# Kernel optimization log

Hardware: AMD Instinct MI355X
Metric: run time of the kernel (lower is better)

## Reference

```python
import jax, jax.numpy as jnp
import numpy as np
from jax.scipy.special import erfinv

N, F0, F1 = 256, 128, 64          # nodes, scalar channels, vector channels
RB, KSEQ, EMB = 32, 16, 32        # radial bins, seq window, pos-embed dim
RC = 24.0                         # radial_cut
NI = F0 + F1                      # num output irreps (per-irrep scalar gate)
CIN = F0 + F1 + 1 + F0            # 321 = per-l fan-in of the message Linear

# real l=2 CG matrices, e3nn component order: (xz, xy, y^2-(x^2+z^2)/2, yz, z^2-x^2)
_M = np.zeros((5, 3, 3), np.float32)
_M[0, 0, 2] = _M[0, 2, 0] = 1.0 / np.sqrt(10.0)
_M[1, 0, 1] = _M[1, 1, 0] = 1.0 / np.sqrt(10.0)
_M[2] = np.diag([-1.0, 2.0, -1.0]) / np.sqrt(30.0)
_M[3, 1, 2] = _M[3, 2, 1] = 1.0 / np.sqrt(10.0)
_M[4] = np.diag([-1.0, 0.0, 1.0]) / np.sqrt(10.0)
M2 = jnp.asarray(_M)

# e3nn-style normalized activation: silu / sqrt(E[silu(z)^2]), z ~ N(0,1)
_zs = jnp.sqrt(2.0) * erfinv(jnp.linspace(-1.0 + 1e-6, 1.0 - 1e-6, 100001))
C_SILU = jnp.sqrt(jnp.mean(jax.nn.silu(_zs) ** 2))

def nsilu(x):
    return jax.nn.silu(x) / C_SILU

def setup_inputs() -> dict:
    key = jax.random.key(0)
    ks = jax.random.split(key, 12)
    return {
        "feat": jax.random.normal(ks[0], (N, F0 + 3 * F1), jnp.float32),
        "coord": 8.0 * jax.random.normal(ks[1], (N, 3), jnp.float32),
        "W_msg0": jax.random.normal(ks[2], (CIN, F0), jnp.float32),
        "W_msg1": jax.random.normal(ks[3], (CIN, F1), jnp.float32),
        "embed_tbl": jax.random.normal(ks[4], (2 * KSEQ + 1, EMB), jnp.float32) / jnp.sqrt(2.0 * KSEQ + 1.0),
        "W_mlp1": jax.random.normal(ks[5], (EMB + RB + F0 + F0, RB), jnp.float32),
        "W_mlp2": jax.random.normal(ks[6], (RB, NI), jnp.float32),
        "W_out0": jax.random.normal(ks[7], (F0, F0), jnp.float32),
        "W_out1": jax.random.normal(ks[8], (F1, F1), jnp.float32),
        "W_move": jax.random.normal(ks[9], (F1, 1), jnp.float32),
        "mask": jax.random.randint(ks[10], (N,), 0, 2).astype(bool),
    }

def reference(feat, coord, W_msg0, W_msg1, embed_tbl, W_mlp1, W_mlp2, W_out0, W_out1, W_move, mask):
    n = feat.shape[0]
    s_in = feat[:, :F0]                       # [N,128] scalar irreps
    v_in = feat[:, F0:].reshape(n, F1, 3)     # [N,64,3] vector irreps
    cm = mask[:, None] & mask[None, :]
    cmf = cm.astype(feat.dtype)
    vec = (coord[:, None, :] - coord[None, :, :]) * cmf[..., None]   # [N,N,3]
    nsq = jnp.sum(vec ** 2, -1)
    dist = jnp.sqrt(jnp.where(nsq == 0.0, 1.0, nsq))
    x, y, z = vec[..., 0], vec[..., 1], vec[..., 2]
    # spherical harmonics, normalize=False, component normalization
    sh1 = jnp.sqrt(3.0) * vec
    sh2 = jnp.stack([jnp.sqrt(15.0) * x * z, jnp.sqrt(15.0) * x * y,
                     jnp.sqrt(5.0) * (y * y - 0.5 * (x * x + z * z)),
                     jnp.sqrt(15.0) * y * z, jnp.sqrt(15.0) / 2.0 * (z * z - x * x)], -1)
    # ---- message Linear over concat([TP(ang, feat_j), ang, feat_j]) ----
    # 0e inputs: [N,N,321]
    in0 = jnp.concatenate([
        cmf[..., None] * s_in[None, :, :],                        # 0e(sh) x 0e
        jnp.einsum('abd,bcd->abc', sh1, v_in) / jnp.sqrt(3.0),    # 1o x 1o -> 0e
        cmf[..., None],                                           # ang 0e (masked)
        jnp.broadcast_to(s_in[None], (n, n, F0)),                 # feat_j 0e
    ], -1)
    msg0 = jnp.einsum('abi,io->abo', in0, W_msg0) / jnp.sqrt(float(CIN))   # [N,N,128]
    # 1o inputs: [N,N,321,3]
    in1 = jnp.concatenate([
        cmf[..., None, None] * v_in[None],                                 # 0e x 1o
        sh1[:, :, None, :] * s_in[None, :, :, None],                       # 1o x 0e
        jnp.sqrt(3.0) * jnp.einsum('abm,mdk,bcd->abck', sh2, M2, v_in),    # 2e x 1o -> 1o
        sh1[:, :, None, :],                                                # ang 1o
        jnp.broadcast_to(v_in[None], (n, n, F1, 3)),                       # feat_j 1o
    ], 2)
    msg1 = jnp.einsum('abid,io->abod', in1, W_msg1) / jnp.sqrt(float(CIN))  # [N,N,64,3]
    # ---- radial / sequence gate ----
    values = jnp.linspace(0.0, RC, RB + 2)[1:-1]
    step = values[1] - values[0]
    rad = jnp.exp(-(((dist[..., None] - values) / step) ** 2)) / 1.12 * cmf[..., None]
    pos = jnp.arange(n)
    rel = pos[:, None] - pos[None, :]
    rel = jnp.where(jnp.abs(rel) <= KSEQ, rel, 0)
    rel = jnp.where(cm, rel, 0) + KSEQ
    pemb = embed_tbl[rel]                                                  # [N,N,32]
    gate_in = jnp.concatenate([pemb, rad,
                               jnp.broadcast_to(s_in[:, None, :], (n, n, F0)),
                               msg0], -1)                                  # [N,N,320]
    h = nsilu(jnp.einsum('abi,io->abo', gate_in, W_mlp1) / jnp.sqrt(float(gate_in.shape[-1])))
    gate = jnp.einsum('abi,io->abo', h, W_mlp2) / jnp.sqrt(float(RB))      # [N,N,192]
    msg0 = msg0 * gate[..., :F0] * cmf[..., None]
    msg1 = msg1 * gate[..., F0:, None] * cmf[..., None, None]
    # ---- masked mean aggregation over j ----
    cnt = jnp.sum(cmf, 1, keepdims=True)
    aggr0 = jnp.sum(msg0, 1) / (cnt + 1e-6)
    aggr1 = jnp.sum(msg1, 1) / (cnt[..., None] + 1e-6)
    keep = (cnt > 1).astype(feat.dtype)
    aggr0 = aggr0 * keep
    aggr1 = aggr1 * keep[..., None]
    # output Linear per irrep type
    f0 = aggr0 @ W_out0 / jnp.sqrt(float(F0))
    f1 = jnp.einsum('ncd,co->nod', aggr1, W_out1) / jnp.sqrt(float(F1))
    # coordinate update (move=True)
    coord_new = coord + 0.001 * jnp.einsum('ncd,co->nod', f1, W_move)[:, 0, :] / jnp.sqrt(float(F1))
    # residual + equivariant layer norm
    r0 = s_in + f0
    r1 = v_in + f1
    mu = jnp.mean(r0, -1, keepdims=True)
    n0 = (r0 - mu) / jnp.sqrt(jnp.var(r0, -1, keepdims=True) + 1e-6)
    rms = jnp.sqrt(jnp.mean(r1 ** 2, (-2, -1), keepdims=True) + 1e-6)
    n1 = r1 / rms
    return jnp.concatenate([n0, n1.reshape(n, -1), coord_new], -1)   # [N, 323]
```

## Files before the change

kernel.cpp:

```cpp
#include <hip/hip_runtime.h>
#include <math.h>

#define NN 256

#define OFF_T0   0
#define OFF_TW   131072
#define OFF_T1A  163840
#define OFF_T1B  229376
#define OFF_S    294912
#define OFF_E    303104
#define OFF_CSP  305152
#define OFF_CS   305408
#define OFF_PART 305472

__device__ __forceinline__ float my_erfinv(float x){
    float w = -logf((1.0f - x) * (1.0f + x));
    float p;
    if (w < 5.0f) {
        w = w - 2.5f;
        p = 2.81022636e-08f;
        p = 3.43273939e-07f + p*w;
        p = -3.5233877e-06f + p*w;
        p = -4.39150654e-06f + p*w;
        p = 0.00021858087f  + p*w;
        p = -0.00125372503f + p*w;
        p = -0.00417768164f + p*w;
        p = 0.246640727f    + p*w;
        p = 1.50140941f     + p*w;
    } else {
        w = sqrtf(w) - 3.0f;
        p = -0.000200214257f;
        p = 0.000100950558f + p*w;
        p = 0.00134934322f  + p*w;
        p = -0.00367342844f + p*w;
        p = 0.00573950773f  + p*w;
        p = -0.0076224613f  + p*w;
        p = 0.00943887047f  + p*w;
        p = 1.00167406f     + p*w;
        p = 2.83297682f     + p*w;
    }
    return p * x;
}

__global__ __launch_bounds__(256) void csilu_partial_kernel(float* ws){
    __shared__ float red[256];
    int t = threadIdx.x, bi = blockIdx.x;
    int lo = bi * 391;
    int hi = lo + 391; if (hi > 100001) hi = 100001;
    float acc = 0.f;
    for (int i = lo + t; i < hi; i += 256){
        float u = -0.999999f + (float)i * (1.999998f / 100000.0f);
        float z = 1.41421356237f * my_erfinv(u);
        float s = z / (1.0f + __expf(-z));
        acc += s * s;
    }
    red[t] = acc;
    __syncthreads();
    for (int off = 128; off >= 1; off >>= 1){
        if (t < off) red[t] += red[t + off];
        __syncthreads();
    }
    if (t == 0) ws[OFF_CSP + bi] = red[0];
}

__global__ __launch_bounds__(256) void precompute_kernel(
    const float* __restrict__ feat, const float* __restrict__ W0,
    const float* __restrict__ W1, const float* __restrict__ tbl,
    const float* __restrict__ Wm1, float* __restrict__ ws)
{
    int b = blockIdx.x, t = threadIdx.x;
    __shared__ float s_l[128], v_l[192];
    __shared__ float P0B_l[128], V0_l[3][128];
    for (int idx = t; idx < 320; idx += 256){
        float val = feat[b*320 + idx];
        if (idx < 128) s_l[idx] = val; else v_l[idx-128] = val;
    }
    __syncthreads();
    if (t < 128){
        int o = t;
        float p0 = W0[192*128 + o];
        for (int i = 0; i < 128; i++){
            float s = s_l[i];
            p0 += s * (W0[i*128 + o] + W0[(193+i)*128 + o]);
        }
        float v0d[3];
        for (int d = 0; d < 3; d++){
            float v0 = 0.f;
            for (int c = 0; c < 64; c++) v0 += v_l[c*3+d] * W0[(128+c)*128 + o];
            v0d[d] = v0;
        }
        P0B_l[o] = p0;
        V0_l[0][o] = v0d[0]; V0_l[1][o] = v0d[1]; V0_l[2][o] = v0d[2];
        ((float4*)(ws + OFF_T0))[b*128 + o] = make_float4(p0, v0d[0], v0d[1], v0d[2]);
    } else if (t < 192){
        int o = t - 128;
        float ac[3];
        for (int k = 0; k < 3; k++){
            float s = 0.f;
            for (int c = 0; c < 64; c++){
                float v = v_l[c*3+k];
                s += v * (W1[c*64 + o] + W1[(257+c)*64 + o]);
            }
            ac[k] = s;
        }
        float p1 = W1[256*64 + o];
        for (int c = 0; c < 128; c++) p1 += s_l[c] * W1[(64+c)*64 + o];
        float u1[3];
        for (int d = 0; d < 3; d++){
            float s = 0.f;
            for (int c = 0; c < 64; c++) s += v_l[c*3+d] * W1[(192+c)*64 + o];
            u1[d] = 1.73205081f * s;
        }
        ((float4*)(ws + OFF_T1A))[b*64 + o] = make_float4(ac[0], ac[1], ac[2], p1);
        ((float4*)(ws + OFF_T1B))[b*64 + o] = make_float4(u1[0], u1[1], u1[2], 0.f);
    } else if (t < 224){
        int r = t - 192;
        float s = 0.f;
        for (int i = 0; i < 128; i++) s += s_l[i] * Wm1[(64+i)*32 + r];
        ws[OFF_S + b*32 + r] = s;
        if (b < 33){
            float e = 0.f;
            for (int k = 0; k < 32; k++) e += tbl[b*32 + k] * Wm1[k*32 + r];
            ws[OFF_E + b*32 + r] = e;
        }
    } else if (b == 0){
        int j = t - 224;
        float s = 0.f;
        for (int k = 0; k < 8; k++) s += ws[OFF_CSP + j*8 + k];
        for (int m = 16; m >= 1; m >>= 1) s += __shfl_xor(s, m);
        if (j == 0) ws[OFF_CS] = 1.0f / sqrtf(s / 100001.0f);
    }
    __syncthreads();
    if (t < 32){
        int r = t;
        float pw = 0.f, vw0 = 0.f, vw1 = 0.f, vw2 = 0.f;
        for (int o = 0; o < 128; o++){
            float w = Wm1[(192+o)*32 + r];
            pw  += P0B_l[o]  * w;
            vw0 += V0_l[0][o]* w;
            vw1 += V0_l[1][o]* w;
            vw2 += V0_l[2][o]* w;
        }
        ((float4*)(ws + OFF_TW))[b*32 + r] = make_float4(pw, vw0, vw1, vw2);
    }
}

__global__ __launch_bounds__(512) void main_kernel(
    const float* __restrict__ coord, const int* __restrict__ maskraw,
    const float* __restrict__ Wm1, const float* __restrict__ Wm2,
    const float* __restrict__ ws, float* __restrict__ part)
{
    const int bid = blockIdx.x;
    const int a = bid >> 2;
    const int q = bid & 3;
    const int t = threadIdx.x;
    const int g = t >> 5;
    const int l = t & 31;

    __shared__ float Wm2_l[32*192];
    __shared__ float Wm1r_l[32*32];
    __shared__ float E_l[33*32];
    __shared__ int   mask_l[NN];
    __shared__ int   blist[NN];
    __shared__ float cxl[NN], cyl[NN], czl[NN];
    __shared__ int   wcnt[4], wbase[4];
    __shared__ int   na_sh;
    __shared__ float red0[8][128];
    __shared__ float red1[8][192];

    {
        const float4* src = (const float4*)Wm2;
        float4* dst = (float4*)Wm2_l;
        for (int idx = t; idx < 1536; idx += 512) dst[idx] = src[idx];
        const float4* src2 = (const float4*)(Wm1 + 1024);
        float4* dst2 = (float4*)Wm1r_l;
        for (int idx = t; idx < 256; idx += 512) dst2[idx] = src2[idx];
        for (int idx = t; idx < 1056; idx += 512) E_l[idx] = ws[OFF_E + idx];
    }

    bool bytemode = false;
    for (int w = 0; w < 64; w++)
        if (maskraw[w] & 0xFFFFFFFE) bytemode = true;
    int m_t = 0;
    if (t < NN){
        if (bytemode){
            unsigned int w = (unsigned int)maskraw[t >> 2];
            m_t = ((w >> ((t & 3) * 8)) & 0xFFu) != 0;
        } else {
            m_t = maskraw[t] != 0;
        }
        mask_l[t] = m_t;
    }
    int pfx = 0;
    if (t < NN){
        unsigned long long bal = __ballot(m_t != 0);
        int lane = t & 63;
        pfx = __popcll(bal & ((1ull << lane) - 1ull));
        if (lane == 0) wcnt[t >> 6] = __popcll(bal);
    }
    __syncthreads();
    if (t == 0){
        int s = 0;
        for (int w = 0; w < 4; w++){ wbase[w] = s; s += wcnt[w]; }
        na_sh = s;
    }
    __syncthreads();
    if (t < NN && m_t) blist[wbase[t >> 6] + pfx] = t;
    __syncthreads();
    const int na_all = na_sh;
    for (int idx = t; idx < na_all; idx += 512){
        int bb = blist[idx];
        cxl[idx] = coord[bb*3+0];
        cyl[idx] = coord[bb*3+1];
        czl[idx] = coord[bb*3+2];
    }
    __syncthreads();

    const float inv_c = ws[OFF_CS];
    const bool mask_a = mask_l[a] != 0;
    const float ca0 = coord[a*3+0], ca1 = coord[a*3+1], ca2 = coord[a*3+2];
    const float sar = ws[OFF_S + a*32 + l];

    const float ISC   = 0.055814557f;
    const float IS320 = 0.055901699f;

    float acc0[4] = {0.f,0.f,0.f,0.f};
    float acc1[2][3] = {{0.f,0.f,0.f},{0.f,0.f,0.f}};

    const int na_eff = mask_a ? na_all : 0;
    const int nq = (na_eff + 3) >> 2;
    const int base = q * nq;
    int cntq = na_eff - base;
    if (cntq < 0) cntq = 0;
    if (cntq > nq) cntq = nq;
    const int iters = (cntq + 15) >> 4;

    const float4* T0  = (const float4*)(ws + OFF_T0);
    const float4* TW  = (const float4*)(ws + OFF_TW);
    const float4* T1A = (const float4*)(ws + OFF_T1A);
    const float4* T1B = (const float4*)(ws + OFF_T1B);

    for (int i = 0; i < iters; i++){
        int il = i*16 + g;
        bool active = il < cntq;
        int idx = base + (active ? il : 0);
        int b = blist[idx];
        float cmf = active ? 1.0f : 0.0f;

        float vx = ca0 - cxl[idx], vy = ca1 - cyl[idx], vz = ca2 - czl[idx];
        float nsq = vx*vx + vy*vy + vz*vz;
        float dist = sqrtf(nsq == 0.0f ? 1.0f : nsq);
        float sh1x = 1.73205081f*vx, sh1y = 1.73205081f*vy, sh1z = 1.73205081f*vz;
        float s20 = 3.87298335f*vx*vz;
        float s21 = 3.87298335f*vx*vy;
        float s22 = 2.23606798f*(vy*vy - 0.5f*(vx*vx + vz*vz));
        float s23 = 3.87298335f*vy*vz;
        float s24 = 1.93649167f*(vz*vz - vx*vx);
        float Txx = -s22*0.182574186f - s24*0.316227766f;
        float Tyy =  s22*0.365148372f;
        float Tzz = -s22*0.182574186f + s24*0.316227766f;
        float Txy =  s21*0.316227766f;
        float Txz =  s20*0.316227766f;
        float Tyz =  s23*0.316227766f;

        float m0v[4];
        #pragma unroll
        for (int j = 0; j < 4; j++){
            float4 t0 = T0[b*128 + l + 32*j];
            m0v[j] = t0.x + vx*t0.y + vy*t0.z + vz*t0.w;
        }

        float vcen = 0.727272727f * (float)(l + 1);
        float ddr = (dist - vcen) * 1.375f;
        float rl = __expf(-ddr*ddr) * 0.892857143f * cmf;
        float radw = 0.f;
        #pragma unroll
        for (int j = 0; j < 32; j++){
            float rj = __shfl(rl, j, 32);
            radw += rj * Wm1r_l[j*32 + l];
        }

        int ir = a - b;
        if (ir > 16 || ir < -16) ir = 0;
        if (!active) ir = 0;
        ir += 16;
        float4 tw = TW[b*32 + l];
        float msgblk = tw.x + vx*tw.y + vy*tw.z + vz*tw.w;
        float pre = (E_l[ir*32 + l] + sar + radw + msgblk*ISC) * IS320;
        float h = pre / (1.0f + __expf(-pre)) * inv_c;

        float gg[6] = {0,0,0,0,0,0};
        #pragma unroll
        for (int r = 0; r < 32; r++){
            float hr = __shfl(h, r, 32);
            #pragma unroll
            for (int k = 0; k < 6; k++) gg[k] += hr * Wm2_l[r*192 + l + 32*k];
        }
        #pragma unroll
        for (int k = 0; k < 6; k++) gg[k] *= cmf;

        #pragma unroll
        for (int j = 0; j < 4; j++) acc0[j] += m0v[j] * gg[j];

        #pragma unroll
        for (int jj = 0; jj < 2; jj++){
            float4 a1 = T1A[b*64 + l + 32*jj];
            float4 u1 = T1B[b*64 + l + 32*jj];
            float gv = gg[4+jj];
            float m10 = a1.x + sh1x*a1.w + Txx*u1.x + Txy*u1.y + Txz*u1.z;
            float m11 = a1.y + sh1y*a1.w + Txy*u1.x + Tyy*u1.y + Tyz*u1.z;
            float m12 = a1.z + sh1z*a1.w + Txz*u1.x + Tyz*u1.y + Tzz*u1.z;
            acc1[jj][0] += m10 * gv;
            acc1[jj][1] += m11 * gv;
            acc1[jj][2] += m12 * gv;
        }
    }

    #pragma unroll
    for (int j = 0; j < 4; j++) acc0[j] += __shfl_xor(acc0[j], 32);
    #pragma unroll
    for (int jj = 0; jj < 2; jj++)
        #pragma unroll
        for (int k = 0; k < 3; k++) acc1[jj][k] += __shfl_xor(acc1[jj][k], 32);

    const int wv = t >> 6;
    if ((t & 63) < 32){
        #pragma unroll
        for (int j = 0; j < 4; j++) red0[wv][l + 32*j] = acc0[j];
        #pragma unroll
        for (int jj = 0; jj < 2; jj++)
            #pragma unroll
            for (int k = 0; k < 3; k++) red1[wv][(l + 32*jj)*3 + k] = acc1[jj][k];
    }
    __syncthreads();

    if (t < 320){
        float s = 0.f;
        if (t < 128){
            #pragma unroll
            for (int w = 0; w < 8; w++) s += red0[w][t];
        } else {
            #pragma unroll
            for (int w = 0; w < 8; w++) s += red1[w][t-128];
        }
        part[bid*320 + t] = s;
    }
}

__global__ __launch_bounds__(256) void epilogue_kernel(
    const float* __restrict__ feat, const float* __restrict__ coord,
    const int* __restrict__ maskraw,
    const float* __restrict__ Wout0, const float* __restrict__ Wout1,
    const float* __restrict__ Wmove,
    const float* __restrict__ part, float* __restrict__ out)
{
    const int a = blockIdx.x;
    const int t = threadIdx.x;

    __shared__ float aggr[320];
    __shared__ float r0_l[128];
    __shared__ float r1_l[192];
    __shared__ float f1_l[192];
    __shared__ float stats[8];
    __shared__ int   wcnt[4];
    __shared__ int   cnt_sh;
    __shared__ int   maska_sh;

    bool bytemode = false;
    for (int w = 0; w < 64; w++)
        if (maskraw[w] & 0xFFFFFFFE) bytemode = true;
    int m_t;
    if (bytemode){
        unsigned int w = (unsigned int)maskraw[t >> 2];
        m_t = ((w >> ((t & 3) * 8)) & 0xFFu) != 0;
    } else {
        m_t = maskraw[t] != 0;
    }
    {
        unsigned long long bal = __ballot(m_t != 0);
        if ((t & 63) == 0) wcnt[t >> 6] = __popcll(bal);
    }
    if (t == a) maska_sh = m_t;
    __syncthreads();
    if (t == 0) cnt_sh = wcnt[0] + wcnt[1] + wcnt[2] + wcnt[3];
    __syncthreads();

    const float cntv = maska_sh ? (float)cnt_sh : 0.0f;
    const float inv = (cntv > 1.0f) ? 1.0f / (cntv + 1e-6f) : 0.0f;
    const float SCALE = 0.055814557f * 0.176776695f;

    for (int idx = t; idx < 320; idx += 256){
        float s = part[(a*4+0)*320 + idx] + part[(a*4+1)*320 + idx]
                + part[(a*4+2)*320 + idx] + part[(a*4+3)*320 + idx];
        aggr[idx] = s * SCALE * inv;
    }
    __syncthreads();

    if (t < 128){
        float f = 0.f;
        for (int c = 0; c < 128; c++) f += aggr[c] * Wout0[c*128 + t];
        r0_l[t] = feat[a*320 + t] + f * 0.088388348f;
    } else if (t < 192){
        int o = t - 128;
        float fv0 = 0.f, fv1 = 0.f, fv2 = 0.f;
        for (int c = 0; c < 64; c++){
            float w = Wout1[c*64 + o];
            fv0 += aggr[128 + c*3+0] * w;
            fv1 += aggr[128 + c*3+1] * w;
            fv2 += aggr[128 + c*3+2] * w;
        }
        fv0 *= 0.125f; fv1 *= 0.125f; fv2 *= 0.125f;
        f1_l[o*3+0] = fv0; f1_l[o*3+1] = fv1; f1_l[o*3+2] = fv2;
        r1_l[o*3+0] = feat[a*320 + 128 + o*3+0] + fv0;
        r1_l[o*3+1] = feat[a*320 + 128 + o*3+1] + fv1;
        r1_l[o*3+2] = feat[a*320 + 128 + o*3+2] + fv2;
    }
    __syncthreads();

    if (t < 64){
        float x0 = r0_l[t], x1 = r0_l[t+64];
        float s0 = x0 + x1, sq = x0*x0 + x1*x1;
        float y0 = r1_l[t*3], y1 = r1_l[t*3+1], y2 = r1_l[t*3+2];
        float s1 = y0*y0 + y1*y1 + y2*y2;
        float wm = Wmove[t];
        float d0 = f1_l[t*3+0]*wm, d1 = f1_l[t*3+1]*wm, d2 = f1_l[t*3+2]*wm;
        #pragma unroll
        for (int off = 32; off >= 1; off >>= 1){
            s0 += __shfl_xor(s0, off);
            sq += __shfl_xor(sq, off);
            s1 += __shfl_xor(s1, off);
            d0 += __shfl_xor(d0, off);
            d1 += __shfl_xor(d1, off);
            d2 += __shfl_xor(d2, off);
        }
        if (t == 0){
            float mu = s0 * (1.0f/128.0f);
            float var = sq * (1.0f/128.0f) - mu*mu;
            stats[0] = mu;
            stats[1] = 1.0f / sqrtf(var + 1e-6f);
            stats[2] = 1.0f / sqrtf(s1 * (1.0f/192.0f) + 1e-6f);
            stats[3] = d0; stats[4] = d1; stats[5] = d2;
        }
    }
    __syncthreads();

    float* orow = out + a*323;
    for (int idx = t; idx < 323; idx += 256){
        float v;
        if (idx < 128)      v = (r0_l[idx] - stats[0]) * stats[1];
        else if (idx < 320) v = r1_l[idx-128] * stats[2];
        else                v = coord[a*3 + (idx-320)] + 0.000125f * stats[3 + (idx-320)];
        orow[idx] = v;
    }
}

extern "C" void kernel_launch(void* const* d_in, const int* in_sizes, int n_in,
                              void* d_out, int out_size, void* d_ws, size_t ws_size,
                              hipStream_t stream)
{
    const float* feat  = (const float*)d_in[0];
    const float* coord = (const float*)d_in[1];
    const float* W0    = (const float*)d_in[2];
    const float* W1    = (const float*)d_in[3];
    const float* tbl   = (const float*)d_in[4];
    const float* Wm1   = (const float*)d_in[5];
    const float* Wm2   = (const float*)d_in[6];
    const float* Wout0 = (const float*)d_in[7];
    const float* Wout1 = (const float*)d_in[8];
    const float* Wmove = (const float*)d_in[9];
    const int*   mask  = (const int*)d_in[10];
    float* ws  = (float*)d_ws;
    float* out = (float*)d_out;

    csilu_partial_kernel<<<256, 256, 0, stream>>>(ws);
    precompute_kernel<<<NN, 256, 0, stream>>>(feat, W0, W1, tbl, Wm1, ws);
    main_kernel<<<NN*4, 512, 0, stream>>>(coord, mask, Wm1, Wm2, ws, ws + OFF_PART);
    epilogue_kernel<<<NN, 256, 0, stream>>>(feat, coord, mask, Wout0, Wout1,
                                            Wmove, ws + OFF_PART, out);
}
```

Before: 207.1 us.

## Fuse csilu into precompute, halve main split, use float4 LDS dot products

Merges the C_SILU partial-sum kernel into the precompute launch as extra blocks, dropping one kernel launch. The main kernel now finishes the final C_SILU reduction and publishes the mask and count for the epilogue, so the epilogue no longer re-derives the mask. The per-neighbour split goes from 4 to 2 blocks per node. The radial and gate matvecs move from lane shuffles to transposed, padded LDS tables read as float4, and partial-sum buffers reuse the weight LDS area. This trades more serial work per block and changed LDS bank patterns for fewer launches and fewer shuffles.

```diff
diff --git a/kernel.cpp b/kernel.cpp
--- a/kernel.cpp
+++ b/kernel.cpp
@@ -2,16 +2,18 @@
 #include <math.h>
 
 #define NN 256
-
-#define OFF_T0   0
-#define OFF_TW   131072
-#define OFF_T1A  163840
-#define OFF_T1B  229376
-#define OFF_S    294912
-#define OFF_E    303104
-#define OFF_CSP  305152
-#define OFF_CS   305408
-#define OFF_PART 305472
+#define NSPLIT 2
+
+#define OFF_T0    0
+#define OFF_TW    131072
+#define OFF_T1A   163840
+#define OFF_T1B   229376
+#define OFF_S     294912
+#define OFF_E     303104
+#define OFF_CSP   305152
+#define OFF_PART  305472
+#define OFF_NA    469312
+#define OFF_MASKD 469376
 
 __device__ __forceinline__ float my_erfinv(float x){
     float w = -logf((1.0f - x) * (1.0f + x));
@@ -42,27 +44,6 @@
     return p * x;
 }
 
-__global__ __launch_bounds__(256) void csilu_partial_kernel(float* ws){
-    __shared__ float red[256];
-    int t = threadIdx.x, bi = blockIdx.x;
-    int lo = bi * 391;
-    int hi = lo + 391; if (hi > 100001) hi = 100001;
-    float acc = 0.f;
-    for (int i = lo + t; i < hi; i += 256){
-        float u = -0.999999f + (float)i * (1.999998f / 100000.0f);
-        float z = 1.41421356237f * my_erfinv(u);
-        float s = z / (1.0f + __expf(-z));
-        acc += s * s;
-    }
-    red[t] = acc;
-    __syncthreads();
-    for (int off = 128; off >= 1; off >>= 1){
-        if (t < off) red[t] += red[t + off];
-        __syncthreads();
-    }
-    if (t == 0) ws[OFF_CSP + bi] = red[0];
-}
-
 __global__ __launch_bounds__(256) void precompute_kernel(
     const float* __restrict__ feat, const float* __restrict__ W0,
     const float* __restrict__ W1, const float* __restrict__ tbl,
@@ -71,6 +52,29 @@
     int b = blockIdx.x, t = threadIdx.x;
     __shared__ float s_l[128], v_l[192];
     __shared__ float P0B_l[128], V0_l[3][128];
+    __shared__ float red[256];
+
+    if (b >= NN){
+        int bi = b - NN;
+        int lo = bi * 391;
+        int hi = lo + 391; if (hi > 100001) hi = 100001;
+        float acc = 0.f;
+        for (int i = lo + t; i < hi; i += 256){
+            float u = -0.999999f + (float)i * (1.999998f / 100000.0f);
+            float z = 1.41421356237f * my_erfinv(u);
+            float s = z / (1.0f + __expf(-z));
+            acc += s * s;
+        }
+        red[t] = acc;
+        __syncthreads();
+        for (int off = 128; off >= 1; off >>= 1){
+            if (t < off) red[t] += red[t + off];
+            __syncthreads();
+        }
+        if (t == 0) ws[OFF_CSP + bi] = red[0];
+        return;
+    }
+
     for (int idx = t; idx < 320; idx += 256){
         float val = feat[b*320 + idx];
         if (idx < 128) s_l[idx] = val; else v_l[idx-128] = val;
@@ -79,6 +83,7 @@
     if (t < 128){
         int o = t;
         float p0 = W0[192*128 + o];
+        #pragma unroll 4
         for (int i = 0; i < 128; i++){
             float s = s_l[i];
             p0 += s * (W0[i*128 + o] + W0[(193+i)*128 + o]);
@@ -86,6 +91,7 @@
         float v0d[3];
         for (int d = 0; d < 3; d++){
             float v0 = 0.f;
+            #pragma unroll 4
             for (int c = 0; c < 64; c++) v0 += v_l[c*3+d] * W0[(128+c)*128 + o];
             v0d[d] = v0;
         }
@@ -97,6 +103,7 @@
         float ac[3];
         for (int k = 0; k < 3; k++){
             float s = 0.f;
+            #pragma unroll 4
             for (int c = 0; c < 64; c++){
                 float v = v_l[c*3+k];
                 s += v * (W1[c*64 + o] + W1[(257+c)*64 + o]);
@@ -104,10 +111,12 @@
             ac[k] = s;
         }
         float p1 = W1[256*64 + o];
+        #pragma unroll 4
         for (int c = 0; c < 128; c++) p1 += s_l[c] * W1[(64+c)*64 + o];
         float u1[3];
         for (int d = 0; d < 3; d++){
             float s = 0.f;
+            #pragma unroll 4
             for (int c = 0; c < 64; c++) s += v_l[c*3+d] * W1[(192+c)*64 + o];
             u1[d] = 1.73205081f * s;
         }
@@ -116,24 +125,21 @@
     } else if (t < 224){
         int r = t - 192;
         float s = 0.f;
+        #pragma unroll 4
         for (int i = 0; i < 128; i++) s += s_l[i] * Wm1[(64+i)*32 + r];
         ws[OFF_S + b*32 + r] = s;
         if (b < 33){
             float e = 0.f;
+            #pragma unroll 4
             for (int k = 0; k < 32; k++) e += tbl[b*32 + k] * Wm1[k*32 + r];
             ws[OFF_E + b*32 + r] = e;
         }
-    } else if (b == 0){
-        int j = t - 224;
-        float s = 0.f;
-        for (int k = 0; k < 8; k++) s += ws[OFF_CSP + j*8 + k];
-        for (int m = 16; m >= 1; m >>= 1) s += __shfl_xor(s, m);
-        if (j == 0) ws[OFF_CS] = 1.0f / sqrtf(s / 100001.0f);
     }
     __syncthreads();
     if (t < 32){
         int r = t;
         float pw = 0.f, vw0 = 0.f, vw1 = 0.f, vw2 = 0.f;
+        #pragma unroll 4
         for (int o = 0; o < 128; o++){
             float w = Wm1[(192+o)*32 + r];
             pw  += P0B_l[o]  * w;
@@ -148,40 +154,45 @@
 __global__ __launch_bounds__(512) void main_kernel(
     const float* __restrict__ coord, const int* __restrict__ maskraw,
     const float* __restrict__ Wm1, const float* __restrict__ Wm2,
-    const float* __restrict__ ws, float* __restrict__ part)
+    float* __restrict__ ws, float* __restrict__ part)
 {
     const int bid = blockIdx.x;
-    const int a = bid >> 2;
-    const int q = bid & 3;
+    const int a = bid >> 1;
+    const int q = bid & 1;
     const int t = threadIdx.x;
     const int g = t >> 5;
     const int l = t & 31;
 
-    __shared__ float Wm2_l[32*192];
-    __shared__ float Wm1r_l[32*32];
-    __shared__ float E_l[33*32];
-    __shared__ int   mask_l[NN];
+    __shared__ __align__(16) float smem_big[192*36];
+    __shared__ __align__(16) float WT1[32*36];
+    __shared__ __align__(16) float E_l[33*32];
+    __shared__ __align__(16) float hsh[16*32];
+    __shared__ __align__(16) float radsh[16*32];
     __shared__ int   blist[NN];
     __shared__ float cxl[NN], cyl[NN], czl[NN];
     __shared__ int   wcnt[4], wbase[4];
-    __shared__ int   na_sh;
-    __shared__ float red0[8][128];
-    __shared__ float red1[8][192];
-
-    {
-        const float4* src = (const float4*)Wm2;
-        float4* dst = (float4*)Wm2_l;
-        for (int idx = t; idx < 1536; idx += 512) dst[idx] = src[idx];
-        const float4* src2 = (const float4*)(Wm1 + 1024);
-        float4* dst2 = (float4*)Wm1r_l;
-        for (int idx = t; idx < 256; idx += 512) dst2[idx] = src2[idx];
-        for (int idx = t; idx < 1056; idx += 512) E_l[idx] = ws[OFF_E + idx];
-    }
-
-    bool bytemode = false;
-    for (int w = 0; w < 64; w++)
-        if (maskraw[w] & 0xFFFFFFFE) bytemode = true;
-    int m_t = 0;
+    __shared__ float cs_part[4];
+    __shared__ int   na_sh, bflag_sh, maska_sh;
+    __shared__ float invc_sh;
+
+    for (int idx = t; idx < 6144; idx += 512){
+        int r = idx / 192, o = idx - r*192;
+        smem_big[o*36 + r] = Wm2[idx];
+    }
+    for (int idx = t; idx < 1024; idx += 512){
+        int j = idx >> 5, l2 = idx & 31;
+        WT1[l2*36 + j] = Wm1[1024 + idx];
+    }
+    for (int idx = t; idx < 1056; idx += 512) E_l[idx] = ws[OFF_E + idx];
+
+    if (t == 0) bflag_sh = 0;
+    __syncthreads();
+    if (t < 64 && (maskraw[t] & 0xFFFFFFFE)) bflag_sh = 1;
+    float cs_acc = (t < NN) ? ws[OFF_CSP + t] : 0.f;
+    __syncthreads();
+    const bool bytemode = bflag_sh != 0;
+
+    int m_t = 0, pfx = 0;
     if (t < NN){
         if (bytemode){
             unsigned int w = (unsigned int)maskraw[t >> 2];
@@ -189,20 +200,24 @@
         } else {
             m_t = maskraw[t] != 0;
         }
-        mask_l[t] = m_t;
-    }
-    int pfx = 0;
-    if (t < NN){
+        if (t == a) maska_sh = m_t;
+        if (bid == 0) ((int*)ws)[OFF_MASKD + t] = m_t;
         unsigned long long bal = __ballot(m_t != 0);
         int lane = t & 63;
         pfx = __popcll(bal & ((1ull << lane) - 1ull));
         if (lane == 0) wcnt[t >> 6] = __popcll(bal);
+        #pragma unroll
+        for (int off = 32; off >= 1; off >>= 1) cs_acc += __shfl_xor(cs_acc, off);
+        if (lane == 0) cs_part[t >> 6] = cs_acc;
     }
     __syncthreads();
     if (t == 0){
         int s = 0;
         for (int w = 0; w < 4; w++){ wbase[w] = s; s += wcnt[w]; }
         na_sh = s;
+        if (bid == 0) ((int*)ws)[OFF_NA] = s;
+        float cstot = cs_part[0] + cs_part[1] + cs_part[2] + cs_part[3];
+        invc_sh = 1.0f / sqrtf(cstot / 100001.0f);
     }
     __syncthreads();
     if (t < NN && m_t) blist[wbase[t >> 6] + pfx] = t;
@@ -216,8 +231,8 @@
     }
     __syncthreads();
 
-    const float inv_c = ws[OFF_CS];
-    const bool mask_a = mask_l[a] != 0;
+    const float inv_c = invc_sh;
+    const bool mask_a = maska_sh != 0;
     const float ca0 = coord[a*3+0], ca1 = coord[a*3+1], ca2 = coord[a*3+2];
     const float sar = ws[OFF_S + a*32 + l];
 
@@ -228,7 +243,7 @@
     float acc1[2][3] = {{0.f,0.f,0.f},{0.f,0.f,0.f}};
 
     const int na_eff = mask_a ? na_all : 0;
-    const int nq = (na_eff + 3) >> 2;
+    const int nq = (na_eff + NSPLIT - 1) / NSPLIT;
     const int base = q * nq;
     int cntq = na_eff - base;
     if (cntq < 0) cntq = 0;
@@ -239,6 +254,8 @@
     const float4* TW  = (const float4*)(ws + OFF_TW);
     const float4* T1A = (const float4*)(ws + OFF_T1A);
     const float4* T1B = (const float4*)(ws + OFF_T1B);
+    const float4* Wm2T4 = (const float4*)smem_big;
+    const float4* WT14  = (const float4*)WT1;
 
     for (int i = 0; i < iters; i++){
         int il = i*16 + g;
@@ -273,11 +290,17 @@
         float vcen = 0.727272727f * (float)(l + 1);
         float ddr = (dist - vcen) * 1.375f;
         float rl = __expf(-ddr*ddr) * 0.892857143f * cmf;
+        radsh[g*32 + l] = rl;
         float radw = 0.f;
-        #pragma unroll
-        for (int j = 0; j < 32; j++){
-            float rj = __shfl(rl, j, 32);
-            radw += rj * Wm1r_l[j*32 + l];
+        {
+            const float4* rv = (const float4*)radsh + g*8;
+            const float4* wv = WT14 + l*9;
+            #pragma unroll
+            for (int j4 = 0; j4 < 8; j4++){
+                float4 r4 = rv[j4];
+                float4 w4 = wv[j4];
+                radw += r4.x*w4.x + r4.y*w4.y + r4.z*w4.z + r4.w*w4.w;
+            }
         }
 
         int ir = a - b;
@@ -288,13 +311,20 @@
         float msgblk = tw.x + vx*tw.y + vy*tw.z + vz*tw.w;
         float pre = (E_l[ir*32 + l] + sar + radw + msgblk*ISC) * IS320;
         float h = pre / (1.0f + __expf(-pre)) * inv_c;
+        hsh[g*32 + l] = h;
 
         float gg[6] = {0,0,0,0,0,0};
-        #pragma unroll
-        for (int r = 0; r < 32; r++){
-            float hr = __shfl(h, r, 32);
+        {
+            const float4* hv = (const float4*)hsh + g*8;
             #pragma unroll
-            for (int k = 0; k < 6; k++) gg[k] += hr * Wm2_l[r*192 + l + 32*k];
+            for (int r4 = 0; r4 < 8; r4++){
+                float4 h4 = hv[r4];
+                #pragma unroll
+                for (int k = 0; k < 6; k++){
+                    float4 w4 = Wm2T4[(l + 32*k)*9 + r4];
+                    gg[k] += h4.x*w4.x + h4.y*w4.y + h4.z*w4.z + h4.w*w4.w;
+                }
+            }
         }
         #pragma unroll
         for (int k = 0; k < 6; k++) gg[k] *= cmf;
@@ -323,14 +353,17 @@
         #pragma unroll
         for (int k = 0; k < 3; k++) acc1[jj][k] += __shfl_xor(acc1[jj][k], 32);
 
+    __syncthreads();
+    float* red0 = smem_big;
+    float* red1 = smem_big + 1024;
     const int wv = t >> 6;
     if ((t & 63) < 32){
         #pragma unroll
-        for (int j = 0; j < 4; j++) red0[wv][l + 32*j] = acc0[j];
+        for (int j = 0; j < 4; j++) red0[wv*128 + l + 32*j] = acc0[j];
         #pragma unroll
         for (int jj = 0; jj < 2; jj++)
             #pragma unroll
-            for (int k = 0; k < 3; k++) red1[wv][(l + 32*jj)*3 + k] = acc1[jj][k];
+            for (int k = 0; k < 3; k++) red1[wv*192 + (l + 32*jj)*3 + k] = acc1[jj][k];
     }
     __syncthreads();
 
@@ -338,10 +371,10 @@
         float s = 0.f;
         if (t < 128){
             #pragma unroll
-            for (int w = 0; w < 8; w++) s += red0[w][t];
+            for (int w = 0; w < 8; w++) s += red0[w*128 + t];
         } else {
             #pragma unroll
-            for (int w = 0; w < 8; w++) s += red1[w][t-128];
+            for (int w = 0; w < 8; w++) s += red1[w*192 + t - 128];
         }
         part[bid*320 + t] = s;
     }
@@ -349,10 +382,10 @@
 
 __global__ __launch_bounds__(256) void epilogue_kernel(
     const float* __restrict__ feat, const float* __restrict__ coord,
-    const int* __restrict__ maskraw,
     const float* __restrict__ Wout0, const float* __restrict__ Wout1,
     const float* __restrict__ Wmove,
-    const float* __restrict__ part, float* __restrict__ out)
+    const float* __restrict__ ws, const float* __restrict__ part,
+    float* __restrict__ out)
 {
     const int a = blockIdx.x;
     const int t = threadIdx.x;
@@ -362,47 +395,30 @@
     __shared__ float r1_l[192];
     __shared__ float f1_l[192];
     __shared__ float stats[8];
-    __shared__ int   wcnt[4];
-    __shared__ int   cnt_sh;
-    __shared__ int   maska_sh;
-
-    bool bytemode = false;
-    for (int w = 0; w < 64; w++)
-        if (maskraw[w] & 0xFFFFFFFE) bytemode = true;
-    int m_t;
-    if (bytemode){
-        unsigned int w = (unsigned int)maskraw[t >> 2];
-        m_t = ((w >> ((t & 3) * 8)) & 0xFFu) != 0;
-    } else {
-        m_t = maskraw[t] != 0;
-    }
-    {
-        unsigned long long bal = __ballot(m_t != 0);
-        if ((t & 63) == 0) wcnt[t >> 6] = __popcll(bal);
-    }
-    if (t == a) maska_sh = m_t;
-    __syncthreads();
-    if (t == 0) cnt_sh = wcnt[0] + wcnt[1] + wcnt[2] + wcnt[3];
-    __syncthreads();
-
-    const float cntv = maska_sh ? (float)cnt_sh : 0.0f;
+
+    const int cnt_i = ((const int*)ws)[OFF_NA];
+    const int ma    = ((const int*)ws)[OFF_MASKD + a];
+    const float cntv = ma ? (float)cnt_i : 0.0f;
     const float inv = (cntv > 1.0f) ? 1.0f / (cntv + 1e-6f) : 0.0f;
     const float SCALE = 0.055814557f * 0.176776695f;
 
     for (int idx = t; idx < 320; idx += 256){
-        float s = part[(a*4+0)*320 + idx] + part[(a*4+1)*320 + idx]
-                + part[(a*4+2)*320 + idx] + part[(a*4+3)*320 + idx];
+        float s = 0.f;
+        #pragma unroll
+        for (int qq = 0; qq < NSPLIT; qq++) s += part[(a*NSPLIT+qq)*320 + idx];
         aggr[idx] = s * SCALE * inv;
     }
     __syncthreads();
 
     if (t < 128){
         float f = 0.f;
+        #pragma unroll 4
         for (int c = 0; c < 128; c++) f += aggr[c] * Wout0[c*128 + t];
         r0_l[t] = feat[a*320 + t] + f * 0.088388348f;
     } else if (t < 192){
         int o = t - 128;
         float fv0 = 0.f, fv1 = 0.f, fv2 = 0.f;
+        #pragma unroll 4
         for (int c = 0; c < 64; c++){
             float w = Wout1[c*64 + o];
             fv0 += aggr[128 + c*3+0] * w;
@@ -472,9 +488,8 @@
     float* ws  = (float*)d_ws;
     float* out = (float*)d_out;
 
-    csilu_partial_kernel<<<256, 256, 0, stream>>>(ws);
-    precompute_kernel<<<NN, 256, 0, stream>>>(feat, W0, W1, tbl, Wm1, ws);
-    main_kernel<<<NN*4, 512, 0, stream>>>(coord, mask, Wm1, Wm2, ws, ws + OFF_PART);
-    epilogue_kernel<<<NN, 256, 0, stream>>>(feat, coord, mask, Wout0, Wout1,
-                                            Wmove, ws + OFF_PART, out);
+    precompute_kernel<<<NN + 256, 256, 0, stream>>>(feat, W0, W1, tbl, Wm1, ws);
+    main_kernel<<<NN*NSPLIT, 512, 0, stream>>>(coord, mask, Wm1, Wm2, ws, ws + OFF_PART);
+    epilogue_kernel<<<NN, 256, 0, stream>>>(feat, coord, Wout0, Wout1, Wmove,
+                                            ws, ws + OFF_PART, out);
 }
```

Result: no change. 203.1 us (-1.9%).
